# Kernel optimization log

Hardware: AMD Instinct MI355X
Metric: run time of the kernel (lower is better)

## Reference

```python
import jax, jax.numpy as jnp
import numpy as np

B, N, D = 4096, 8192, 512
MARGIN = 1.0


def setup_inputs() -> dict:
    key = jax.random.key(0)
    k1, k2, k3 = jax.random.split(key, 3)
    anchor = jax.random.normal(k1, (B, D), dtype=jnp.float32)
    sample = jax.random.normal(k2, (N, D), dtype=jnp.float32)
    # L2-normalize: the module uses 1 - dot as a cosine-style distance
    anchor = anchor / jnp.linalg.norm(anchor, axis=1, keepdims=True)
    sample = sample / jnp.linalg.norm(sample, axis=1, keepdims=True)
    # one-hot positive label per anchor row (docstring: one-hot LongTensor)
    pos_pos = jax.random.randint(k3, (B,), 0, N)
    positive_idx = jax.nn.one_hot(pos_pos, N, dtype=jnp.int64)
    return {"anchor_features": anchor, "sample_features": sample,
            "positive_idx": positive_idx}


def reference(anchor_features, sample_features, positive_idx):
    # distances: [B, N]
    dist = 1.0 - jnp.matmul(anchor_features, sample_features.T)
    pos_mask = positive_idx.astype(bool)
    # exactly one positive per row -> pos_dist: [B]
    pos_dist = jnp.sum(jnp.where(pos_mask, dist, 0.0), axis=1)
    # hinge against every negative (num_neg=0, smooth=False branch)
    hinge = jnp.maximum(pos_dist[:, None] - dist + MARGIN, 0.0)  # [B, N]
    per_row = jnp.sum(jnp.where(pos_mask, 0.0, hinge), axis=1) / (N - 1)
    # losses summed over batch, then averaged (average=True)
    return jnp.mean(per_row)
```

## Files before the change

kernel.cpp:

```cpp
#include <hip/hip_runtime.h>
#include <stdint.h>

#define M_ROWS 4096
#define N_COLS 8192
#define KDIM   512

#define BM 256
#define BN 256
#define BKT 32
#define NKT 16

typedef __attribute__((ext_vector_type(4))) float  f32x4;
typedef __attribute__((ext_vector_type(4))) int    i32x4;

#define BAR() do { asm volatile("" ::: "memory"); \
                   __builtin_amdgcn_s_barrier();  \
                   asm volatile("" ::: "memory"); } while (0)

__device__ __forceinline__ unsigned int cvt4_fp8(float4 v) {
  int r = 0;
  r = __builtin_amdgcn_cvt_pk_fp8_f32(v.x, v.y, r, false);
  r = __builtin_amdgcn_cvt_pk_fp8_f32(v.z, v.w, r, true);
  return (unsigned int)r;
}

__global__ __launch_bounds__(256) void prep_kernel(
    const float* __restrict__ A, const float* __restrict__ S,
    const int* __restrict__ onehot,
    unsigned char* __restrict__ A8, unsigned char* __restrict__ S8,
    int* __restrict__ pos_idx) {
  const int b = blockIdx.x, tid = threadIdx.x;

  #pragma unroll
  for (int i = 0; i < 2; ++i) {
    int li = tid + i * 256;
    if (li < 384) {
      int idx = b * 384 + li;
      if (idx < 524288) {
        float4 v = reinterpret_cast<const float4*>(A)[idx];
        reinterpret_cast<unsigned int*>(A8)[idx] = cvt4_fp8(v);
      } else {
        int q = idx - 524288;
        float4 v = reinterpret_cast<const float4*>(S)[q];
        reinterpret_cast<unsigned int*>(S8)[q] = cvt4_fp8(v);
      }
    }
  }

  const i32x4* row = reinterpret_cast<const i32x4*>(onehot + (size_t)b * N_COLS);
  #pragma unroll
  for (int i = 0; i < 8; ++i) {
    i32x4 v = __builtin_nontemporal_load(&row[i * 256 + tid]);
    if (v[0] | v[1] | v[2] | v[3]) {
      int j = (i * 256 + tid) * 4 + (v[0] ? 0 : (v[1] ? 1 : (v[2] ? 2 : 3)));
      pos_idx[b] = j;
    }
  }
}

__device__ __forceinline__ int x1(int r) { return (r >> 2) & 1; }

__device__ __forceinline__ long lds_frag8(const unsigned char* chunk, int r, int q) {
  int byt = r * 32 + (((q >> 1) ^ x1(r)) * 16) + (q & 1) * 8;
  return *reinterpret_cast<const long*>(chunk + byt);
}

__device__ __forceinline__ void stage_chunk8(const unsigned char* __restrict__ srcBase,
                                             int tt, unsigned char* chunk, int tid) {
  int r = tid >> 1, h = tid & 1;
  const unsigned char* src = srcBase + (size_t)r * KDIM + tt * BKT + (h ^ x1(r)) * 16;
  __builtin_amdgcn_global_load_lds(
      (const __attribute__((address_space(1))) void*)src,
      (__attribute__((address_space(3))) void*)(chunk + tid * 16),
      16, 0, 0);
}

template<int T>
__device__ __forceinline__ void do_tile(unsigned char (*lds)[2][BM * BKT],
                                        const unsigned char* __restrict__ Abase,
                                        const unsigned char* __restrict__ Sbase,
                                        f32x4 (&acc)[8][4],
                                        int wr, int wc, int lr, int lk, int tid) {
  constexpr bool STAGE = (T <= NKT - 4);
  const unsigned char* cA = lds[T & 3][0];
  const unsigned char* cB = lds[T & 3][1];

  long bfr[4], afr[4];
  #pragma unroll
  for (int n = 0; n < 4; ++n) bfr[n] = lds_frag8(cB, wc * 64 + n * 16 + lr, lk);
  #pragma unroll
  for (int m = 0; m < 4; ++m) afr[m] = lds_frag8(cA, wr * 128 + m * 16 + lr, lk);
  if constexpr (STAGE) stage_chunk8(Abase, T + 3, lds[(T + 3) & 3][0], tid);
  BAR();
  __builtin_amdgcn_s_setprio(1);
  #pragma unroll
  for (int m = 0; m < 4; ++m)
    #pragma unroll
    for (int n = 0; n < 4; ++n)
      acc[m][n] = __builtin_amdgcn_mfma_f32_16x16x32_fp8_fp8(afr[m], bfr[n],
                                                             acc[m][n], 0, 0, 0);
  __builtin_amdgcn_s_setprio(0);
  BAR();
  #pragma unroll
  for (int m = 0; m < 4; ++m) afr[m] = lds_frag8(cA, wr * 128 + (m + 4) * 16 + lr, lk);
  if constexpr (STAGE) stage_chunk8(Sbase, T + 3, lds[(T + 3) & 3][1], tid);
  BAR();
  __builtin_amdgcn_s_setprio(1);
  #pragma unroll
  for (int m = 0; m < 4; ++m)
    #pragma unroll
    for (int n = 0; n < 4; ++n)
      acc[m + 4][n] = __builtin_amdgcn_mfma_f32_16x16x32_fp8_fp8(afr[m], bfr[n],
                                                                 acc[m + 4][n], 0, 0, 0);
  __builtin_amdgcn_s_setprio(0);
  if constexpr (T <= 12)      asm volatile("s_waitcnt vmcnt(4)" ::: "memory");
  else if constexpr (T == 13) asm volatile("s_waitcnt vmcnt(2)" ::: "memory");
  else if constexpr (T == 14) asm volatile("s_waitcnt vmcnt(0)" ::: "memory");
  BAR();
}

__global__ __launch_bounds__(512, 2) void gemm_kernel(
    const unsigned char* __restrict__ A8,
    const unsigned char* __restrict__ S8,
    float* __restrict__ rsum, float* __restrict__ rmin) {
  __shared__ alignas(16) unsigned char lds[4][2][BM * BKT];
  const int tid  = threadIdx.x;
  const int bx   = blockIdx.x;
  const int wg   = ((bx & 7) << 6) | (bx >> 3);
  const int w    = tid >> 6;
  const int lane = tid & 63;
  const int wr   = w >> 2, wc = w & 3;
  const int lr   = lane & 15, lk = lane >> 4;
  const int rp   = wg & 15, cp = wg >> 4;
  const int rowBase = rp * BM;

  const unsigned char* Abase = A8 + (size_t)rowBase * KDIM;
  const unsigned char* Sbase = S8 + (size_t)cp * BN * KDIM;

  f32x4 acc[8][4];
  #pragma unroll
  for (int m = 0; m < 8; ++m)
    #pragma unroll
    for (int n = 0; n < 4; ++n)
      acc[m][n] = (f32x4){0.f, 0.f, 0.f, 0.f};

  #pragma unroll
  for (int tt = 0; tt < 3; ++tt) {
    stage_chunk8(Abase, tt, lds[tt][0], tid);
    stage_chunk8(Sbase, tt, lds[tt][1], tid);
  }
  asm volatile("s_waitcnt vmcnt(4)" ::: "memory");
  BAR();

  do_tile<0>(lds, Abase, Sbase, acc, wr, wc, lr, lk, tid);
  do_tile<1>(lds, Abase, Sbase, acc, wr, wc, lr, lk, tid);
  do_tile<2>(lds, Abase, Sbase, acc, wr, wc, lr, lk, tid);
  do_tile<3>(lds, Abase, Sbase, acc, wr, wc, lr, lk, tid);
  do_tile<4>(lds, Abase, Sbase, acc, wr, wc, lr, lk, tid);
  do_tile<5>(lds, Abase, Sbase, acc, wr, wc, lr, lk, tid);
  do_tile<6>(lds, Abase, Sbase, acc, wr, wc, lr, lk, tid);
  do_tile<7>(lds, Abase, Sbase, acc, wr, wc, lr, lk, tid);
  do_tile<8>(lds, Abase, Sbase, acc, wr, wc, lr, lk, tid);
  do_tile<9>(lds, Abase, Sbase, acc, wr, wc, lr, lk, tid);
  do_tile<10>(lds, Abase, Sbase, acc, wr, wc, lr, lk, tid);
  do_tile<11>(lds, Abase, Sbase, acc, wr, wc, lr, lk, tid);
  do_tile<12>(lds, Abase, Sbase, acc, wr, wc, lr, lk, tid);
  do_tile<13>(lds, Abase, Sbase, acc, wr, wc, lr, lk, tid);
  do_tile<14>(lds, Abase, Sbase, acc, wr, wc, lr, lk, tid);
  do_tile<15>(lds, Abase, Sbase, acc, wr, wc, lr, lk, tid);
  __syncthreads();

  float* eps = (float*)&lds[0][0][0];
  float* epm = eps + 4096;
  #pragma unroll
  for (int m = 0; m < 8; ++m)
    #pragma unroll
    for (int r = 0; r < 4; ++r) {
      float s_ = (acc[m][0][r] + acc[m][1][r]) + (acc[m][2][r] + acc[m][3][r]);
      float n_ = fminf(fminf(acc[m][0][r], acc[m][1][r]),
                       fminf(acc[m][2][r], acc[m][3][r]));
      s_ += __shfl_xor(s_, 4, 64);
      n_ = fminf(n_, __shfl_xor(n_, 4, 64));
      s_ += __shfl_xor(s_, 8, 64);
      n_ = fminf(n_, __shfl_xor(n_, 8, 64));
      if ((lane & 12) == 0) {
        int row = wr * 128 + m * 16 + lk * 4 + r;
        int cls = lane & 3;
        eps[(row * 4 + cls) * 4 + wc] = s_;
        epm[(row * 4 + cls) * 4 + wc] = n_;
      }
    }
  __syncthreads();
  #pragma unroll
  for (int item = tid; item < 1024; item += 512) {
    int row = item >> 2, cls = item & 3;
    float s0 = (eps[item * 4 + 0] + eps[item * 4 + 1]) +
               (eps[item * 4 + 2] + eps[item * 4 + 3]);
    float m0 = fminf(fminf(epm[item * 4 + 0], epm[item * 4 + 1]),
                     fminf(epm[item * 4 + 2], epm[item * 4 + 3]));
    size_t gi = (size_t)(rowBase + row) * 128 + cp * 4 + cls;
    rsum[gi] = s0;
    rmin[gi] = m0;
  }
}

__global__ __launch_bounds__(256) void fin1_kernel(
    const float* __restrict__ A, const float* __restrict__ Sm,
    const int* __restrict__ pos_idx,
    const float* __restrict__ rsum, const float* __restrict__ rmin,
    float* __restrict__ rowLoss) {
  const int w = threadIdx.x >> 6, lane = threadIdx.x & 63;
  #pragma unroll
  for (int i = 0; i < 2; ++i) {
    int row = blockIdx.x * 8 + w * 2 + i;
    int j = pos_idx[row];
    const float4* a4 = reinterpret_cast<const float4*>(A + (size_t)row * KDIM);
    const float4* s4 = reinterpret_cast<const float4*>(Sm + (size_t)j * KDIM);
    float4 x0 = a4[lane * 2], x1_ = a4[lane * 2 + 1];
    float4 y0 = s4[lane * 2], y1_ = s4[lane * 2 + 1];
    float dp = x0.x * y0.x + x0.y * y0.y + x0.z * y0.z + x0.w * y0.w
             + x1_.x * y1_.x + x1_.y * y1_.y + x1_.z * y1_.z + x1_.w * y1_.w;
    float rs = rsum[(size_t)row * 128 + lane] + rsum[(size_t)row * 128 + 64 + lane];
    float rm = fminf(rmin[(size_t)row * 128 + lane],
                     rmin[(size_t)row * 128 + 64 + lane]);
    #pragma unroll
    for (int off = 32; off > 0; off >>= 1) {
      dp += __shfl_down(dp, off, 64);
      rs += __shfl_down(rs, off, 64);
      rm = fminf(rm, __shfl_down(rm, off, 64));
    }
    float p  = __shfl(dp, 0, 64);
    float R  = __shfl(rs, 0, 64);
    float mn = __shfl(rm, 0, 64);
    float loss;
    if (mn >= p - 1.0f) {
      loss = (R - p) - (float)(N_COLS - 1) * (p - 1.0f);
    } else {
      float accv = 0.f;
      const float* arow = A + (size_t)row * KDIM;
      for (int n = lane; n < N_COLS; n += 64) {
        const float* srow = Sm + (size_t)n * KDIM;
        float d = 0.f;
        for (int k = 0; k < KDIM; ++k) d += arow[k] * srow[k];
        float h = fmaxf(d - p + 1.0f, 0.0f);
        accv += (n == j) ? 0.f : h;
      }
      #pragma unroll
      for (int off = 32; off > 0; off >>= 1) accv += __shfl_down(accv, off, 64);
      loss = __shfl(accv, 0, 64);
    }
    if (lane == 0) rowLoss[row] = loss;
  }
}

__global__ __launch_bounds__(256) void fin2_kernel(const float* __restrict__ rowLoss,
                                                   float* __restrict__ out) {
  __shared__ double sd[256];
  double s = 0.0;
  for (int i = threadIdx.x; i < M_ROWS; i += 256) s += (double)rowLoss[i];
  sd[threadIdx.x] = s;
  __syncthreads();
  for (int st = 128; st > 0; st >>= 1) {
    if (threadIdx.x < st) sd[threadIdx.x] += sd[threadIdx.x + st];
    __syncthreads();
  }
  if (threadIdx.x == 0)
    *out = (float)(sd[0] / ((double)M_ROWS * (double)(N_COLS - 1)));
}

extern "C" void kernel_launch(void* const* d_in, const int* in_sizes, int n_in,
                              void* d_out, int out_size, void* d_ws, size_t ws_size,
                              hipStream_t stream) {
  const float* A  = (const float*)d_in[0];
  const float* S  = (const float*)d_in[1];
  const int*   oh = (const int*)d_in[2];
  float* out = (float*)d_out;

  char* ws = (char*)d_ws;
  int*   pos_idx  = (int*)ws;
  float* rsum     = (float*)(ws + 16384);
  float* rmin     = (float*)(ws + 16384 + 2097152);
  float* rowLoss  = (float*)(ws + 16384 + 4194304);
  unsigned char* A8 = (unsigned char*)(ws + 16384 + 4194304 + 16384);
  unsigned char* S8 = A8 + (size_t)M_ROWS * KDIM;

  prep_kernel<<<M_ROWS, 256, 0, stream>>>(A, S, oh, A8, S8, pos_idx);
  gemm_kernel<<<512, 512, 0, stream>>>(A8, S8, rsum, rmin);
  fin1_kernel<<<512, 256, 0, stream>>>(A, S, pos_idx, rsum, rmin, rowLoss);
  fin2_kernel<<<1, 256, 0, stream>>>(rowLoss, out);
}
```

Baseline: 78.04 us.

## Overlap one-hot positive scan with fp8 GEMM via interleaved scan blocks

```diff
diff --git a/kernel.cpp b/kernel.cpp
--- a/kernel.cpp
+++ b/kernel.cpp
@@ -24,36 +24,21 @@
   return (unsigned int)r;
 }
 
-__global__ __launch_bounds__(256) void prep_kernel(
-    const float* __restrict__ A, const float* __restrict__ S,
-    const int* __restrict__ onehot,
-    unsigned char* __restrict__ A8, unsigned char* __restrict__ S8,
-    int* __restrict__ pos_idx) {
-  const int b = blockIdx.x, tid = threadIdx.x;
-
-  #pragma unroll
-  for (int i = 0; i < 2; ++i) {
-    int li = tid + i * 256;
-    if (li < 384) {
-      int idx = b * 384 + li;
-      if (idx < 524288) {
-        float4 v = reinterpret_cast<const float4*>(A)[idx];
-        reinterpret_cast<unsigned int*>(A8)[idx] = cvt4_fp8(v);
-      } else {
-        int q = idx - 524288;
-        float4 v = reinterpret_cast<const float4*>(S)[q];
-        reinterpret_cast<unsigned int*>(S8)[q] = cvt4_fp8(v);
-      }
-    }
-  }
-
-  const i32x4* row = reinterpret_cast<const i32x4*>(onehot + (size_t)b * N_COLS);
-  #pragma unroll
-  for (int i = 0; i < 8; ++i) {
-    i32x4 v = __builtin_nontemporal_load(&row[i * 256 + tid]);
-    if (v[0] | v[1] | v[2] | v[3]) {
-      int j = (i * 256 + tid) * 4 + (v[0] ? 0 : (v[1] ? 1 : (v[2] ? 2 : 3)));
-      pos_idx[b] = j;
+__global__ __launch_bounds__(256) void cvt_kernel(const float* __restrict__ A,
+                                                  const float* __restrict__ S,
+                                                  unsigned char* __restrict__ A8,
+                                                  unsigned char* __restrict__ S8) {
+  int g = blockIdx.x * 256 + threadIdx.x;
+  #pragma unroll
+  for (int it = 0; it < 4; ++it) {
+    int idx = g + it * 393216;
+    if (idx < 524288) {
+      float4 v = reinterpret_cast<const float4*>(A)[idx];
+      reinterpret_cast<unsigned int*>(A8)[idx] = cvt4_fp8(v);
+    } else {
+      int q = idx - 524288;
+      float4 v = reinterpret_cast<const float4*>(S)[q];
+      reinterpret_cast<unsigned int*>(S8)[q] = cvt4_fp8(v);
     }
   }
 }
@@ -119,14 +104,36 @@
   BAR();
 }
 
-__global__ __launch_bounds__(512, 2) void gemm_kernel(
+__global__ __launch_bounds__(512, 2) void gemm_scan_kernel(
     const unsigned char* __restrict__ A8,
     const unsigned char* __restrict__ S8,
+    const int* __restrict__ onehot,
+    int* __restrict__ pos_idx,
     float* __restrict__ rsum, float* __restrict__ rmin) {
   __shared__ alignas(16) unsigned char lds[4][2][BM * BKT];
   const int tid  = threadIdx.x;
   const int bx   = blockIdx.x;
-  const int wg   = ((bx & 7) << 6) | (bx >> 3);
+
+  if ((bx % 5) == 4) {
+    const int s = bx / 5;
+    const i32x4* base = reinterpret_cast<const i32x4*>(onehot + (size_t)s * 32 * N_COLS);
+    #pragma unroll 1
+    for (int r = 0; r < 32; ++r) {
+      const i32x4* rowp = base + (size_t)r * 2048;
+      #pragma unroll
+      for (int i = 0; i < 4; ++i) {
+        i32x4 v = __builtin_nontemporal_load(&rowp[i * 512 + tid]);
+        if (v[0] | v[1] | v[2] | v[3]) {
+          int j = (i * 512 + tid) * 4 + (v[0] ? 0 : (v[1] ? 1 : (v[2] ? 2 : 3)));
+          pos_idx[s * 32 + r] = j;
+        }
+      }
+    }
+    return;
+  }
+
+  const int g    = bx - (bx + 1) / 5;
+  const int wg   = ((g & 7) << 6) | (g >> 3);
   const int w    = tid >> 6;
   const int lane = tid & 63;
   const int wr   = w >> 2, wc = w & 3;
@@ -284,8 +291,8 @@
   unsigned char* A8 = (unsigned char*)(ws + 16384 + 4194304 + 16384);
   unsigned char* S8 = A8 + (size_t)M_ROWS * KDIM;
 
-  prep_kernel<<<M_ROWS, 256, 0, stream>>>(A, S, oh, A8, S8, pos_idx);
-  gemm_kernel<<<512, 512, 0, stream>>>(A8, S8, rsum, rmin);
+  cvt_kernel<<<1536, 256, 0, stream>>>(A, S, A8, S8);
+  gemm_scan_kernel<<<640, 512, 0, stream>>>(A8, S8, oh, pos_idx, rsum, rmin);
   fin1_kernel<<<512, 256, 0, stream>>>(A, S, pos_idx, rsum, rmin, rowLoss);
   fin2_kernel<<<1, 256, 0, stream>>>(rowLoss, out);
 }
```

Measured after the change: 135.6 us. 73.8% more time.
